# Kernel optimization log

Hardware: AMD Instinct MI355X
Metric: run time of the kernel (lower is better)

## Reference

```python
import jax, jax.numpy as jnp
import numpy as np

# Config constants (match init_kwargs)
N_EXPERTS = 8
CAPACITY = 1280
W_IMPORTANCE = 0.01
W_LOAD = 0.01
LAMBDA_Z = 0.001
W_PENALTY = 0.01


def setup_inputs() -> dict:
    key = jax.random.key(0)
    ks = jax.random.split(key, 6)
    B, T, C, E, F = 4, 2048, 1024, N_EXPERTS, 4096
    s = 0.02
    return {
        "x": jax.random.normal(ks[0], (B, T, C), dtype=jnp.float32),
        "gate_w": jax.random.normal(ks[1], (E, C), dtype=jnp.float32) * s,
        "gate_b": jnp.zeros((E,), dtype=jnp.float32),
        "w1": jax.random.normal(ks[2], (E, F, C), dtype=jnp.float32) * s,
        "b1": jnp.zeros((E, F), dtype=jnp.float32),
        "w2": jax.random.normal(ks[3], (E, C, F), dtype=jnp.float32) * s,
        "b2": jnp.zeros((E, C), dtype=jnp.float32),
    }


def reference(x, gate_w, gate_b, w1, b1, w2, b2):
    B, T, C = x.shape
    E = N_EXPERTS
    xf = x.reshape(B * T, C)
    bt = xf.shape[0]

    # ---- routing ----
    gate_logits = xf @ gate_w.T + gate_b  # (BT, E)

    # penalty loss
    p = jax.nn.softmax(gate_logits / 1.66, axis=-1)
    pen_a = jnp.mean(p * (1.0 - p))
    pm = p.mean(axis=0)
    pen_b = 1.0 / E - jnp.mean(pm * (1.0 - pm))
    penalty = W_PENALTY * (pen_a + pen_b)

    # z-loss
    z_loss = LAMBDA_Z * jnp.mean(jax.nn.logsumexp(gate_logits, axis=-1) ** 2)

    router_probs = jax.nn.softmax(gate_logits.astype(jnp.float32), axis=-1).astype(x.dtype)
    top1_idx = jnp.argmax(router_probs, axis=-1)        # (BT,)
    top1_w = jnp.max(router_probs, axis=-1)             # (BT,)
    onehot = jax.nn.one_hot(top1_idx, E, dtype=jnp.int32)

    # capacity masking: position of each token within its chosen expert
    priority = jnp.cumsum(onehot, axis=0)               # (BT, E)
    pos = priority[jnp.arange(bt), top1_idx] - 1        # (BT,)
    keep = pos < CAPACITY                               # (BT,) bool

    # load-balance loss
    f_i = onehot.astype(x.dtype).mean(axis=0)
    P_i = router_probs.mean(axis=0)
    load_loss = W_LOAD * E * jnp.sum(f_i * P_i)

    # importance loss (scatter of top1 probs == onehot-weighted sum)
    importance = (onehot.astype(x.dtype) * top1_w[:, None]).sum(axis=0)  # (E,)
    cv2 = jnp.var(importance) / jnp.mean(importance) ** 2
    importance_loss = W_IMPORTANCE * cv2

    aux_loss = penalty + z_loss + load_loss + importance_loss

    # ---- dispatch -> grouped FFN -> combine ----
    pos_c = jnp.clip(pos, 0, CAPACITY - 1)
    keep_f = keep.astype(x.dtype)[:, None]
    buf = jnp.zeros((E, CAPACITY, C), dtype=x.dtype).at[top1_idx, pos_c].add(xf * keep_f)
    h = jax.nn.gelu(jnp.einsum('ekc,efc->ekf', buf, w1) + b1[:, None, :], approximate=True)
    yb = jnp.einsum('ekf,ecf->ekc', h, w2) + b2[:, None, :]
    y = yb[top1_idx, pos_c] * keep_f                    # dropped tokens -> 0

    out = (top1_w[:, None] * y).reshape(B, T, C)
    return out, aux_loss
```

## Files before the change

### kernel.cpp

```cpp
#include <hip/hip_runtime.h>
#include <hip/hip_bf16.h>
#include <stdint.h>

#define BTOK 8192
#define CDIM 1024
#define NEXP 8
#define FDIM 4096
#define ECAP 1280

typedef __attribute__((ext_vector_type(8))) unsigned short u16x8;
typedef __attribute__((ext_vector_type(8))) __bf16 bf16x8;
typedef __attribute__((ext_vector_type(4))) float f32x4;

__device__ __forceinline__ unsigned short f2bf(float f) {
    unsigned int u = __builtin_bit_cast(unsigned int, f);
    u += 0x7FFFu + ((u >> 16) & 1u);
    return (unsigned short)(u >> 16);
}

__device__ __forceinline__ bf16x8 lds_load8(const unsigned short* p) {
    return __builtin_bit_cast(bf16x8, *(const u16x8*)p);
}

__device__ __forceinline__ float gelu_tanh(float v) {
    float u = 0.7978845608028654f * (v + 0.044715f * v * v * v);
    float e = __expf(2.0f * u);
    float t = 1.0f - 2.0f * __builtin_amdgcn_rcpf(e + 1.0f);
    return 0.5f * v * (1.0f + t);
}

__device__ __forceinline__ void glds16(const unsigned short* g, unsigned short* l) {
    __builtin_amdgcn_global_load_lds(
        (const __attribute__((address_space(1))) void*)g,
        (__attribute__((address_space(3))) void*)l,
        16, 0, 0);
}

__device__ __forceinline__ void stage_tile(
    const unsigned short* const* gA, const unsigned short* const* gB,
    unsigned short* As, unsigned short* Bs, int wbase, int koff)
{
#pragma unroll
    for (int j = 0; j < 4; j++) {
        glds16(gA[j] + koff, As + j * 2048 + wbase);
        glds16(gB[j] + koff, Bs + j * 2048 + wbase);
    }
}

__device__ __forceinline__ void mfma_tile(
    const unsigned short* As, const unsigned short* Bs,
    int wm, int wn, int fr, int kq, int sw, f32x4 acc[4][4])
{
#pragma unroll
    for (int kk = 0; kk < 64; kk += 32) {
        bf16x8 af[4], bfr[4];
#pragma unroll
        for (int i = 0; i < 4; i++) {
            af[i]  = lds_load8(&As[(wm * 64 + i * 16 + fr) * 64 + ((kk + kq) ^ sw)]);
            bfr[i] = lds_load8(&Bs[(wn * 64 + i * 16 + fr) * 64 + ((kk + kq) ^ sw)]);
        }
#pragma unroll
        for (int i = 0; i < 4; i++)
#pragma unroll
            for (int j = 0; j < 4; j++)
                acc[i][j] = __builtin_amdgcn_mfma_f32_16x16x32_bf16(af[i], bfr[j], acc[i][j], 0, 0, 0);
    }
}

__global__ __launch_bounds__(256) void cvt_kernel(
    const float* __restrict__ src, unsigned short* __restrict__ dst, int n8)
{
    int i = blockIdx.x * 256 + threadIdx.x;
    if (i >= n8) return;
    const float4* s = (const float4*)(src + (size_t)i * 8);
    float4 a = s[0], b = s[1];
    u16x8 o;
    o[0] = f2bf(a.x); o[1] = f2bf(a.y); o[2] = f2bf(a.z); o[3] = f2bf(a.w);
    o[4] = f2bf(b.x); o[5] = f2bf(b.y); o[6] = f2bf(b.z); o[7] = f2bf(b.w);
    *(u16x8*)(dst + (size_t)i * 8) = o;
}

__global__ __launch_bounds__(256) void gate_kernel(
    const float* __restrict__ x,
    const float* __restrict__ gw,
    const float* __restrict__ gb,
    float* __restrict__ logits,
    unsigned short* __restrict__ xb)
{
    const int lane = threadIdx.x & 63;
    const int wave = threadIdx.x >> 6;
    const int tok = blockIdx.x * 4 + wave;
    const float* xr = x + (size_t)tok * CDIM + lane * 16;
    float xv[16];
#pragma unroll
    for (int j = 0; j < 4; j++) {
        float4 v = ((const float4*)xr)[j];
        xv[4 * j] = v.x; xv[4 * j + 1] = v.y; xv[4 * j + 2] = v.z; xv[4 * j + 3] = v.w;
    }
    u16x8 o0, o1;
#pragma unroll
    for (int j = 0; j < 8; j++) o0[j] = f2bf(xv[j]);
#pragma unroll
    for (int j = 0; j < 8; j++) o1[j] = f2bf(xv[8 + j]);
    unsigned short* xo = xb + (size_t)tok * CDIM + lane * 16;
    *(u16x8*)xo = o0;
    *(u16x8*)(xo + 8) = o1;

    float acc[8];
#pragma unroll
    for (int e = 0; e < 8; e++) {
        const float* wr = gw + e * CDIM + lane * 16;
        float s = 0.f;
#pragma unroll
        for (int j = 0; j < 4; j++) {
            float4 v = ((const float4*)wr)[j];
            s += xv[4 * j] * v.x + xv[4 * j + 1] * v.y + xv[4 * j + 2] * v.z + xv[4 * j + 3] * v.w;
        }
        acc[e] = s;
    }
#pragma unroll
    for (int e = 0; e < 8; e++) {
#pragma unroll
        for (int off = 32; off > 0; off >>= 1)
            acc[e] += __shfl_xor(acc[e], off);
    }
    if (lane == 0) {
#pragma unroll
        for (int e = 0; e < 8; e++)
            logits[(size_t)tok * 8 + e] = acc[e] + gb[e];
    }
}

__global__ __launch_bounds__(256) void route_kernel(
    const float* __restrict__ logits,
    int* __restrict__ top1i, float* __restrict__ top1w,
    int* __restrict__ toks, float* __restrict__ slotw,
    int* __restrict__ cnt, float* __restrict__ aux_out)
{
    const int tid = threadIdx.x;
    const int TPT = BTOK / 256;
    float psum[8] = {}, qsum[8] = {}, imp[8] = {};
    int cnte[8] = {};
    float pen_a_s = 0.f, z_s = 0.f;
    const float INV_T = 1.0f / 1.66f;

    for (int i = 0; i < TPT; i++) {
        int t = tid * TPT + i;
        float l[8];
#pragma unroll
        for (int e = 0; e < 8; e++) l[e] = logits[t * 8 + e];
        float m = l[0];
#pragma unroll
        for (int e = 1; e < 8; e++) m = fmaxf(m, l[e]);
        float ex[8], se = 0.f;
#pragma unroll
        for (int e = 0; e < 8; e++) { ex[e] = __expf(l[e] - m); se += ex[e]; }
        float inv = 1.0f / se;
#pragma unroll
        for (int e = 0; e < 8; e++) psum[e] += ex[e] * inv;
        int am = 0; float bl = l[0];
#pragma unroll
        for (int e = 1; e < 8; e++) if (l[e] > bl) { bl = l[e]; am = e; }
        float w = ex[am] * inv;
        imp[am] += w; cnte[am]++;
        top1i[t] = am; top1w[t] = w;
        float lse = m + __logf(se);
        z_s += lse * lse;
        float m2 = m * INV_T, se2 = 0.f, ex2[8];
#pragma unroll
        for (int e = 0; e < 8; e++) { ex2[e] = __expf(l[e] * INV_T - m2); se2 += ex2[e]; }
        float inv2 = 1.0f / se2;
#pragma unroll
        for (int e = 0; e < 8; e++) { float q = ex2[e] * inv2; pen_a_s += q * (1.f - q); qsum[e] += q; }
    }

    __shared__ int sc[256][8];
#pragma unroll
    for (int e = 0; e < 8; e++) sc[tid][e] = cnte[e];
    __syncthreads();
    for (int st = 1; st < 256; st <<= 1) {
        int v[8];
        bool act = (tid >= st);
        if (act) {
#pragma unroll
            for (int e = 0; e < 8; e++) v[e] = sc[tid - st][e];
        }
        __syncthreads();
        if (act) {
#pragma unroll
            for (int e = 0; e < 8; e++) sc[tid][e] += v[e];
        }
        __syncthreads();
    }
    int run[8], tot[8];
#pragma unroll
    for (int e = 0; e < 8; e++) {
        run[e] = (tid > 0) ? sc[tid - 1][e] : 0;
        tot[e] = sc[255][e];
    }
    for (int i = 0; i < TPT; i++) {
        int t = tid * TPT + i;
        int am = top1i[t];
        int pos = 0;
#pragma unroll
        for (int e = 0; e < 8; e++) if (e == am) pos = run[e]++;
        if (pos < ECAP) {
            toks[am * ECAP + pos] = t;
            slotw[am * ECAP + pos] = top1w[t];
        }
    }
    if (tid < 8) cnt[tid] = (tot[tid] < ECAP) ? tot[tid] : ECAP;

    __shared__ float red[26][256];
    red[0][tid] = pen_a_s;
    red[1][tid] = z_s;
#pragma unroll
    for (int e = 0; e < 8; e++) {
        red[2 + e][tid] = qsum[e];
        red[10 + e][tid] = psum[e];
        red[18 + e][tid] = imp[e];
    }
    __syncthreads();
    for (int st = 128; st > 0; st >>= 1) {
        if (tid < st) {
#pragma unroll
            for (int j = 0; j < 26; j++) red[j][tid] += red[j][tid + st];
        }
        __syncthreads();
    }
    if (tid == 0) {
        const float BTf = (float)BTOK;
        float pen_a = red[0][0] / (BTf * 8.f);
        float pb = 0.f;
        for (int e = 0; e < 8; e++) { float pm = red[2 + e][0] / BTf; pb += pm * (1.f - pm); }
        float pen_b = 0.125f - pb * 0.125f;
        float penalty = 0.01f * (pen_a + pen_b);
        float z = 0.001f * red[1][0] / BTf;
        float load = 0.f;
        for (int e = 0; e < 8; e++) load += ((float)tot[e] / BTf) * (red[10 + e][0] / BTf);
        load *= 0.01f * 8.f;
        float mu = 0.f;
        for (int e = 0; e < 8; e++) mu += red[18 + e][0];
        mu *= 0.125f;
        float var = 0.f;
        for (int e = 0; e < 8; e++) { float d = red[18 + e][0] - mu; var += d * d; }
        var *= 0.125f;
        float cv2 = var / (mu * mu);
        float aux = penalty + z + load + 0.01f * cv2;
        aux_out[0] = aux;
    }
}

__global__ __launch_bounds__(256) void ffn1_kernel(
    const unsigned short* __restrict__ xb,
    const unsigned short* __restrict__ w1b,
    const float* __restrict__ b1,
    const int* __restrict__ toks,
    const int* __restrict__ cnt,
    unsigned short* __restrict__ H)
{
    const int e = blockIdx.y;
    const int MT = ECAP / 128;
    const int nbq = (int)gridDim.x >> 3;
    const int bid = blockIdx.x;
    const int b2 = (bid & 7) * nbq + (bid >> 3);
    const int mt = b2 % MT;
    const int nt = b2 / MT;
    const int cnt_e = cnt[e];
    const int m0 = mt * 128;
    if (m0 >= cnt_e) return;
    const int n0 = nt * 128;
    const unsigned short* W = w1b + (size_t)e * FDIM * CDIM;
    const int* tk = toks + e * ECAP;

    __shared__ __align__(16) unsigned short As[2 * 128 * 64];
    __shared__ __align__(16) unsigned short Bs[2 * 128 * 64];

    const int tid = threadIdx.x;
    const int lane = tid & 63;
    const int wave = tid >> 6;
    const int wm = wave & 1;
    const int wn = wave >> 1;
    const int wbase = wave * 512;

    const unsigned short* gA[4];
    const unsigned short* gB[4];
#pragma unroll
    for (int j = 0; j < 4; j++) {
        int idx = j * 256 + tid;
        int r = idx >> 3;
        int ch = (idx & 7) ^ (r & 7);
        int row = m0 + r;
        int tokid = (row < cnt_e) ? tk[row] : 0;
        if ((unsigned)tokid >= BTOK) tokid = 0;
        gA[j] = xb + (size_t)tokid * CDIM + ch * 8;
        gB[j] = W + (size_t)(n0 + r) * CDIM + ch * 8;
    }
    f32x4 acc[4][4] = {};
    const int fr = lane & 15;
    const int kq = (lane >> 4) * 8;
    const int sw = (fr & 7) << 3;

    stage_tile(gA, gB, As, Bs, wbase, 0);
    __syncthreads();

    const int NT = CDIM / 64;
#pragma unroll 1
    for (int t = 0; t < NT; t += 2) {
        if (t + 1 < NT) stage_tile(gA, gB, As + 8192, Bs + 8192, wbase, (t + 1) * 64);
        mfma_tile(As, Bs, wm, wn, fr, kq, sw, acc);
        __syncthreads();
        if (t + 2 < NT) stage_tile(gA, gB, As, Bs, wbase, (t + 2) * 64);
        mfma_tile(As + 8192, Bs + 8192, wm, wn, fr, kq, sw, acc);
        __syncthreads();
    }
    const int cq = (lane >> 4) * 4;
#pragma unroll
    for (int i = 0; i < 4; i++) {
#pragma unroll
        for (int j = 0; j < 4; j++) {
            int n = n0 + wn * 64 + j * 16 + fr;
            float bias = b1[e * FDIM + n];
            size_t base = ((size_t)e * ECAP + (m0 + wm * 64 + i * 16 + cq)) * FDIM + n;
#pragma unroll
            for (int rr = 0; rr < 4; rr++) {
                float v = acc[i][j][rr] + bias;
                H[base + (size_t)rr * FDIM] = f2bf(gelu_tanh(v));
            }
        }
    }
}

__global__ __launch_bounds__(256) void ffn2_kernel(
    const unsigned short* __restrict__ H,
    const unsigned short* __restrict__ w2b,
    const float* __restrict__ b2,
    const int* __restrict__ toks,
    const float* __restrict__ slotw,
    const int* __restrict__ cnt,
    float* __restrict__ out)
{
    const int e = blockIdx.y;
    const int MT = ECAP / 128;
    const int nbq = (int)gridDim.x >> 3;
    const int bid = blockIdx.x;
    const int b2i = (bid & 7) * nbq + (bid >> 3);
    const int mt = b2i % MT;
    const int nt = b2i / MT;
    const int cnt_e = cnt[e];
    const int m0 = mt * 128;
    if (m0 >= cnt_e) return;
    const int n0 = nt * 128;
    const unsigned short* W = w2b + (size_t)e * CDIM * FDIM;
    const unsigned short* Hb = H + (size_t)e * ECAP * FDIM;

    __shared__ __align__(16) unsigned short As[2 * 128 * 64];
    __shared__ __align__(16) unsigned short Bs[2 * 128 * 64];

    const int tid = threadIdx.x;
    const int lane = tid & 63;
    const int wave = tid >> 6;
    const int wm = wave & 1;
    const int wn = wave >> 1;
    const int wbase = wave * 512;

    const unsigned short* gA[4];
    const unsigned short* gB[4];
#pragma unroll
    for (int j = 0; j < 4; j++) {
        int idx = j * 256 + tid;
        int r = idx >> 3;
        int ch = (idx & 7) ^ (r & 7);
        gA[j] = Hb + (size_t)(m0 + r) * FDIM + ch * 8;
        gB[j] = W + (size_t)(n0 + r) * FDIM + ch * 8;
    }
    f32x4 acc[4][4] = {};
    const int fr = lane & 15;
    const int kq = (lane >> 4) * 8;
    const int sw = (fr & 7) << 3;

    stage_tile(gA, gB, As, Bs, wbase, 0);
    __syncthreads();

    const int NT = FDIM / 64;
#pragma unroll 1
    for (int t = 0; t < NT; t += 2) {
        if (t + 1 < NT) stage_tile(gA, gB, As + 8192, Bs + 8192, wbase, (t + 1) * 64);
        mfma_tile(As, Bs, wm, wn, fr, kq, sw, acc);
        __syncthreads();
        if (t + 2 < NT) stage_tile(gA, gB, As, Bs, wbase, (t + 2) * 64);
        mfma_tile(As + 8192, Bs + 8192, wm, wn, fr, kq, sw, acc);
        __syncthreads();
    }
    const int cq = (lane >> 4) * 4;
#pragma unroll
    for (int i = 0; i < 4; i++) {
#pragma unroll
        for (int rr = 0; rr < 4; rr++) {
            int s = m0 + wm * 64 + i * 16 + cq + rr;
            if (s < cnt_e) {
                int t = toks[e * ECAP + s];
                float wgt = slotw[e * ECAP + s];
                if ((unsigned)t < BTOK) {
#pragma unroll
                    for (int j = 0; j < 4; j++) {
                        int n = n0 + wn * 64 + j * 16 + fr;
                        float y = acc[i][j][rr] + b2[e * CDIM + n];
                        out[(size_t)t * CDIM + n] = wgt * y;
                    }
                }
            }
        }
    }
}

extern "C" void kernel_launch(void* const* d_in, const int* in_sizes, int n_in,
                              void* d_out, int out_size, void* d_ws, size_t ws_size,
                              hipStream_t stream)
{
    (void)in_sizes; (void)n_in; (void)ws_size;
    const float* x  = (const float*)d_in[0];
    const float* gw = (const float*)d_in[1];
    const float* gb = (const float*)d_in[2];
    const float* w1 = (const float*)d_in[3];
    const float* b1 = (const float*)d_in[4];
    const float* w2 = (const float*)d_in[5];
    const float* b2 = (const float*)d_in[6];
    float* out = (float*)d_out;

    char* ws = (char*)d_ws;
    size_t off = 0;
    unsigned short* H   = (unsigned short*)(ws + off); off += (size_t)NEXP * ECAP * FDIM * 2;
    unsigned short* xb  = (unsigned short*)(ws + off); off += (size_t)BTOK * CDIM * 2;
    unsigned short* w1b = (unsigned short*)(ws + off); off += (size_t)NEXP * FDIM * CDIM * 2;
    unsigned short* w2b = (unsigned short*)(ws + off); off += (size_t)NEXP * CDIM * FDIM * 2;
    float* logits = (float*)(ws + off); off += (size_t)BTOK * 8 * 4;
    int* top1i    = (int*)(ws + off);   off += (size_t)BTOK * 4;
    float* top1w  = (float*)(ws + off); off += (size_t)BTOK * 4;
    int* toks     = (int*)(ws + off);   off += (size_t)NEXP * ECAP * 4;
    float* slotw  = (float*)(ws + off); off += (size_t)NEXP * ECAP * 4;
    int* cnt      = (int*)(ws + off);   off += (size_t)NEXP * 4;

    hipMemsetAsync(d_out, 0, (size_t)out_size * sizeof(float), stream);

    const int NW = NEXP * FDIM * CDIM / 8;
    cvt_kernel<<<(NW + 255) / 256, 256, 0, stream>>>(w1, w1b, NW);
    cvt_kernel<<<(NW + 255) / 256, 256, 0, stream>>>(w2, w2b, NW);

    gate_kernel<<<BTOK / 4, 256, 0, stream>>>(x, gw, gb, logits, xb);
    route_kernel<<<1, 256, 0, stream>>>(logits, top1i, top1w, toks, slotw, cnt,
                                        out + (size_t)BTOK * CDIM);
    ffn1_kernel<<<dim3((ECAP / 128) * (FDIM / 128), NEXP), 256, 0, stream>>>(xb, w1b, b1, toks, cnt, H);
    ffn2_kernel<<<dim3((ECAP / 128) * (CDIM / 128), NEXP), 256, 0, stream>>>(H, w2b, b2, toks, slotw, cnt, out);
}
```

Before: 698.2 us.

## Move per-token softmax and loss statistics from single-block route kernel into gate kernel

Per-token softmax, argmax, z-loss and penalty terms are now computed in the parallel gate kernel, which writes per-block partial sums instead of raw logits. The single-block route kernel then only counts expert assignments, runs the prefix scan, and reduces the 26 partial arrays. This takes serial per-token work out of a one-block kernel that runs on a single CU. The cost is a small extra shared-memory reduction and a block-wide sync in every gate block, and summation order changes slightly.

```diff
diff --git a/kernel.cpp b/kernel.cpp
--- a/kernel.cpp
+++ b/kernel.cpp
@@ -7,6 +7,7 @@
 #define NEXP 8
 #define FDIM 4096
 #define ECAP 1280
+#define NGB (BTOK / 4)
 
 typedef __attribute__((ext_vector_type(8))) unsigned short u16x8;
 typedef __attribute__((ext_vector_type(8))) __bf16 bf16x8;
@@ -84,8 +85,9 @@
     const float* __restrict__ x,
     const float* __restrict__ gw,
     const float* __restrict__ gb,
-    float* __restrict__ logits,
-    unsigned short* __restrict__ xb)
+    unsigned short* __restrict__ xb,
+    int* __restrict__ top1i, float* __restrict__ top1w,
+    float* __restrict__ partials)
 {
     const int lane = threadIdx.x & 63;
     const int wave = threadIdx.x >> 6;
@@ -124,54 +126,66 @@
         for (int off = 32; off > 0; off >>= 1)
             acc[e] += __shfl_xor(acc[e], off);
     }
+    const float INV_T = 1.0f / 1.66f;
+    float l[8];
+#pragma unroll
+    for (int e = 0; e < 8; e++) l[e] = acc[e] + gb[e];
+    float m = l[0];
+#pragma unroll
+    for (int e = 1; e < 8; e++) m = fmaxf(m, l[e]);
+    float ex[8], se = 0.f;
+#pragma unroll
+    for (int e = 0; e < 8; e++) { ex[e] = __expf(l[e] - m); se += ex[e]; }
+    float inv = 1.0f / se;
+    int am = 0; float bl = l[0];
+#pragma unroll
+    for (int e = 1; e < 8; e++) if (l[e] > bl) { bl = l[e]; am = e; }
+    float w = ex[am] * inv;
+    float lse = m + __logf(se);
+    float zz = lse * lse;
+    float m2 = m * INV_T, se2 = 0.f, ex2[8];
+#pragma unroll
+    for (int e = 0; e < 8; e++) { ex2[e] = __expf(l[e] * INV_T - m2); se2 += ex2[e]; }
+    float inv2 = 1.0f / se2;
+    float pen = 0.f, q[8];
+#pragma unroll
+    for (int e = 0; e < 8; e++) { q[e] = ex2[e] * inv2; pen += q[e] * (1.f - q[e]); }
+
+    __shared__ float part[26][4];
     if (lane == 0) {
-#pragma unroll
-        for (int e = 0; e < 8; e++)
-            logits[(size_t)tok * 8 + e] = acc[e] + gb[e];
-    }
+        top1i[tok] = am;
+        top1w[tok] = w;
+        part[0][wave] = pen;
+        part[1][wave] = zz;
+#pragma unroll
+        for (int e = 0; e < 8; e++) {
+            part[2 + e][wave]  = q[e];
+            part[10 + e][wave] = ex[e] * inv;
+            part[18 + e][wave] = (e == am) ? w : 0.f;
+        }
+    }
+    __syncthreads();
+    const int tid = threadIdx.x;
+    if (tid < 26)
+        partials[tid * NGB + blockIdx.x] =
+            part[tid][0] + part[tid][1] + part[tid][2] + part[tid][3];
 }
 
 __global__ __launch_bounds__(256) void route_kernel(
-    const float* __restrict__ logits,
-    int* __restrict__ top1i, float* __restrict__ top1w,
+    const int* __restrict__ top1i, const float* __restrict__ top1w,
+    const float* __restrict__ partials,
     int* __restrict__ toks, float* __restrict__ slotw,
     int* __restrict__ cnt, float* __restrict__ aux_out)
 {
     const int tid = threadIdx.x;
     const int TPT = BTOK / 256;
-    float psum[8] = {}, qsum[8] = {}, imp[8] = {};
+    int ti[TPT];
     int cnte[8] = {};
-    float pen_a_s = 0.f, z_s = 0.f;
-    const float INV_T = 1.0f / 1.66f;
-
+#pragma unroll
     for (int i = 0; i < TPT; i++) {
-        int t = tid * TPT + i;
-        float l[8];
-#pragma unroll
-        for (int e = 0; e < 8; e++) l[e] = logits[t * 8 + e];
-        float m = l[0];
-#pragma unroll
-        for (int e = 1; e < 8; e++) m = fmaxf(m, l[e]);
-        float ex[8], se = 0.f;
-#pragma unroll
-        for (int e = 0; e < 8; e++) { ex[e] = __expf(l[e] - m); se += ex[e]; }
-        float inv = 1.0f / se;
-#pragma unroll
-        for (int e = 0; e < 8; e++) psum[e] += ex[e] * inv;
-        int am = 0; float bl = l[0];
-#pragma unroll
-        for (int e = 1; e < 8; e++) if (l[e] > bl) { bl = l[e]; am = e; }
-        float w = ex[am] * inv;
-        imp[am] += w; cnte[am]++;
-        top1i[t] = am; top1w[t] = w;
-        float lse = m + __logf(se);
-        z_s += lse * lse;
-        float m2 = m * INV_T, se2 = 0.f, ex2[8];
-#pragma unroll
-        for (int e = 0; e < 8; e++) { ex2[e] = __expf(l[e] * INV_T - m2); se2 += ex2[e]; }
-        float inv2 = 1.0f / se2;
-#pragma unroll
-        for (int e = 0; e < 8; e++) { float q = ex2[e] * inv2; pen_a_s += q * (1.f - q); qsum[e] += q; }
+        ti[i] = top1i[tid * TPT + i];
+#pragma unroll
+        for (int e = 0; e < 8; e++) cnte[e] += (ti[i] == e) ? 1 : 0;
     }
 
     __shared__ int sc[256][8];
@@ -198,9 +212,10 @@
         run[e] = (tid > 0) ? sc[tid - 1][e] : 0;
         tot[e] = sc[255][e];
     }
+#pragma unroll
     for (int i = 0; i < TPT; i++) {
         int t = tid * TPT + i;
-        int am = top1i[t];
+        int am = ti[i];
         int pos = 0;
 #pragma unroll
         for (int e = 0; e < 8; e++) if (e == am) pos = run[e]++;
@@ -211,15 +226,16 @@
     }
     if (tid < 8) cnt[tid] = (tot[tid] < ECAP) ? tot[tid] : ECAP;
 
+    float r[26];
+#pragma unroll
+    for (int j = 0; j < 26; j++) {
+        float s = 0.f;
+        for (int i = tid; i < NGB; i += 256) s += partials[j * NGB + i];
+        r[j] = s;
+    }
     __shared__ float red[26][256];
-    red[0][tid] = pen_a_s;
-    red[1][tid] = z_s;
-#pragma unroll
-    for (int e = 0; e < 8; e++) {
-        red[2 + e][tid] = qsum[e];
-        red[10 + e][tid] = psum[e];
-        red[18 + e][tid] = imp[e];
-    }
+#pragma unroll
+    for (int j = 0; j < 26; j++) red[j][tid] = r[j];
     __syncthreads();
     for (int st = 128; st > 0; st >>= 1) {
         if (tid < st) {
@@ -434,7 +450,7 @@
     unsigned short* xb  = (unsigned short*)(ws + off); off += (size_t)BTOK * CDIM * 2;
     unsigned short* w1b = (unsigned short*)(ws + off); off += (size_t)NEXP * FDIM * CDIM * 2;
     unsigned short* w2b = (unsigned short*)(ws + off); off += (size_t)NEXP * CDIM * FDIM * 2;
-    float* logits = (float*)(ws + off); off += (size_t)BTOK * 8 * 4;
+    float* partials = (float*)(ws + off); off += (size_t)26 * NGB * 4;
     int* top1i    = (int*)(ws + off);   off += (size_t)BTOK * 4;
     float* top1w  = (float*)(ws + off); off += (size_t)BTOK * 4;
     int* toks     = (int*)(ws + off);   off += (size_t)NEXP * ECAP * 4;
@@ -447,8 +463,8 @@
     cvt_kernel<<<(NW + 255) / 256, 256, 0, stream>>>(w1, w1b, NW);
     cvt_kernel<<<(NW + 255) / 256, 256, 0, stream>>>(w2, w2b, NW);
 
-    gate_kernel<<<BTOK / 4, 256, 0, stream>>>(x, gw, gb, logits, xb);
-    route_kernel<<<1, 256, 0, stream>>>(logits, top1i, top1w, toks, slotw, cnt,
+    gate_kernel<<<NGB, 256, 0, stream>>>(x, gw, gb, xb, top1i, top1w, partials);
+    route_kernel<<<1, 256, 0, stream>>>(top1i, top1w, partials, toks, slotw, cnt,
                                         out + (size_t)BTOK * CDIM);
     ffn1_kernel<<<dim3((ECAP / 128) * (FDIM / 128), NEXP), 256, 0, stream>>>(xb, w1b, b1, toks, cnt, H);
     ffn2_kernel<<<dim3((ECAP / 128) * (CDIM / 128), NEXP), 256, 0, stream>>>(H, w2b, b2, toks, slotw, cnt, out);
```

New measurement: 723.5 us. 3.6% more time.
